# Kernel tuning notes

Measured on AMD Instinct MI355X. Metric: run time of the kernel, lower is better.

Reference implementation:

```python
import jax, jax.numpy as jnp
import numpy as np

SEQ, DM, NH, DH = 8192, 1024, 16, 64


def setup_inputs() -> dict:
    key = jax.random.key(0)
    k = jax.random.split(key, 8)
    return {
        "xs": jax.random.normal(k[0], (SEQ, DM), dtype=jnp.float32),
        "wq": jax.random.normal(k[1], (NH, DH, DM), dtype=jnp.float32),
        "wk": jax.random.normal(k[2], (NH, DH, DM), dtype=jnp.float32),
        "wv": jax.random.normal(k[3], (NH, DH, DM), dtype=jnp.float32),
        # MLP: Linear(NH*DH -> DM), gelu, Linear(DM -> NH*DH); eqx stores W as (out, in)
        "w1": jax.random.normal(k[4], (DM, NH * DH), dtype=jnp.float32) * 0.02,
        "b1": jnp.zeros((DM,), dtype=jnp.float32),
        "w2": jax.random.normal(k[5], (NH * DH, DM), dtype=jnp.float32) * 0.02,
        "b2": jnp.zeros((NH * DH,), dtype=jnp.float32),
    }


def _act(x):
    return jax.nn.elu(x) + 1.0


def reference(xs, wq, wk, wv, w1, b1, w2, b2):
    # project: (n_heads d_head d_model),(seq d_model) -> (seq n_heads d_head)
    q = jnp.einsum('hdm,sm->shd', wq, xs)
    k = jnp.einsum('hdm,sm->shd', wk, xs)
    v = jnp.einsum('hdm,sm->shd', wv, xs)

    def cell(state, qkv):
        s, z = state                      # s: (h, dk, dv), z: (h, dk)
        qt, kt, vt = qkv                  # each (h, d)
        kt = _act(kt)
        s = s + jnp.einsum('hk,hv->hkv', kt, vt)
        z = z + kt
        qa = _act(qt)
        # faithful to einops 'n_heads d_head_k d_head_v, n_heads d_head_q -> n_heads d_head_v'
        sq = jnp.einsum('hkv,hq->hv', s, qa)
        zq = jnp.einsum('hk,hq->h', z, qa)
        return (s, z), sq / zq[:, None]

    init = (jnp.zeros((NH, DH, DH), xs.dtype), jnp.zeros((NH, DH), xs.dtype))
    _, out = jax.lax.scan(cell, init, (q, k, v))   # out: (seq, h, d)
    out = out.reshape(SEQ, NH * DH)
    h = jax.nn.gelu(out @ w1.T + b1)
    return h @ w2.T + b2
```

## Files before the change

kernel.cpp:

```cpp
#include <hip/hip_runtime.h>
#include <hip/hip_bf16.h>

using bf16 = __hip_bfloat16;
typedef __attribute__((ext_vector_type(8))) short shortx8;
typedef __attribute__((ext_vector_type(4))) float f32x4;

#define SEQ 8192
#define DM 1024
#define NH 16
#define CHUNK 64
#define NC (SEQ / CHUNK)
#define NT (DM / 64)

__device__ __forceinline__ void load_lds16(const bf16* g, bf16* l) {
    __builtin_amdgcn_global_load_lds(
        (const __attribute__((address_space(1))) void*)g,
        (__attribute__((address_space(3))) void*)l, 16, 0, 0);
}

__device__ __forceinline__ unsigned ldsoff(const bf16* p) {
    return (unsigned)(unsigned long long)(__attribute__((address_space(3))) const void*)p;
}

__device__ __forceinline__ shortx8 dsr128(unsigned a) {
    shortx8 r;
    asm volatile("ds_read_b128 %0, %1" : "=v"(r) : "v"(a));
    return r;
}

__device__ __forceinline__ float bf2f(short s) {
    union { unsigned u; float f; } x;
    x.u = ((unsigned)(unsigned short)s) << 16;
    return x.f;
}

__global__ __launch_bounds__(256) void convert_all(const float* __restrict__ xs,
                                                   const float* __restrict__ wk,
                                                   const float* __restrict__ wv,
                                                   const float* __restrict__ w1,
                                                   const float* __restrict__ w2,
                                                   bf16* __restrict__ xsb,
                                                   bf16* __restrict__ wall) {
    const int b = blockIdx.x;
    const float* in;
    bf16* out;
    int blk;
    if (b < 8192) {
        in = xs; out = xsb; blk = b;
    } else {
        const int seg = (b - 8192) >> 10;
        blk = (b - 8192) & 1023;
        out = wall + (size_t)seg * DM * DM;
        if (seg == 0)      in = wk;
        else if (seg == 1) in = wv;
        else if (seg == 2) in = w1;
        else               in = w2;
    }
    size_t i = ((size_t)blk * 256 + threadIdx.x) * 4;
    float4 f = *(const float4*)(in + i);
    out[i + 0] = __float2bfloat16(f.x);
    out[i + 1] = __float2bfloat16(f.y);
    out[i + 2] = __float2bfloat16(f.z);
    out[i + 3] = __float2bfloat16(f.w);
}

__global__ __launch_bounds__(512, 2) void gemm256(const bf16* __restrict__ A,
                                                  const bf16* __restrict__ B,
                                                  void* __restrict__ Cv,
                                                  float* __restrict__ kappa,
                                                  int N) {
    __shared__ __align__(16) bf16 As[2][256][64];
    __shared__ __align__(16) bf16 Bs[2][256][64];

    const int tid = threadIdx.x;
    const int nwg = gridDim.x * gridDim.y;
    const int bid = blockIdx.x + blockIdx.y * gridDim.x;
    const int cpx = nwg >> 3;
    const int swz = (bid & 7) * cpx + (bid >> 3);
    const int ry  = swz % gridDim.y;
    const int rx  = swz / gridDim.y;
    const int bm  = ry * 256;
    const int bn  = rx * 256;

    const int wave = tid >> 6;
    const int lane = tid & 63;
    const int wr   = wave >> 2;
    const int wc   = wave & 3;
    const int quad = lane >> 4;
    const int m16  = lane & 15;
    const int r7   = m16 & 7;
    const int wr128 = wr * 128;
    const int wc64  = wc * 64;
    const int kp0 = ((quad ^ r7) * 8);
    const int kp1 = (((4 + quad) ^ r7) * 8);

    auto stageA = [&](int half, int kt) {
        #pragma unroll
        for (int it = 0; it < 2; ++it) {
            int s = it * 512 + tid;
            int row = s >> 3, pos = s & 7;
            int g = pos ^ (row & 7);
            load_lds16(A + (size_t)(bm + half * 128 + row) * DM + kt * 64 + g * 8,
                       &As[kt & 1][half * 128 + row][pos * 8]);
        }
    };
    auto stageB = [&](int half, int kt) {
        #pragma unroll
        for (int it = 0; it < 2; ++it) {
            int s = it * 512 + tid;
            int row = s >> 3, pos = s & 7;
            int g = pos ^ (row & 7);
            load_lds16(B + (size_t)(bn + half * 128 + row) * DM + kt * 64 + g * 8,
                       &Bs[kt & 1][half * 128 + row][pos * 8]);
        }
    };

    f32x4 acc[8][4];
    #pragma unroll
    for (int i = 0; i < 8; ++i)
        #pragma unroll
        for (int j = 0; j < 4; ++j)
            #pragma unroll
            for (int r = 0; r < 4; ++r) acc[i][j][r] = 0.f;

    stageA(0, 0); stageA(1, 0); stageB(0, 0); stageB(1, 0);
    stageB(0, 1); stageB(1, 1);
    asm volatile("s_waitcnt vmcnt(4)");
    __builtin_amdgcn_s_barrier();

    shortx8 af[4][2], blo[2][2], bhi[2][2];

    #pragma unroll 1
    for (int t = 0; t < NT; ++t) {
        const int sl = t & 1;
        if (t + 1 < NT) { stageA(0, t + 1); stageA(1, t + 1); }
        #pragma unroll
        for (int i = 0; i < 4; ++i) {
            af[i][0] = dsr128(ldsoff(&As[sl][wr128 + i * 16 + m16][kp0]));
            af[i][1] = dsr128(ldsoff(&As[sl][wr128 + i * 16 + m16][kp1]));
        }
        #pragma unroll
        for (int j = 0; j < 2; ++j) {
            blo[j][0] = dsr128(ldsoff(&Bs[sl][wc64 + j * 16 + m16][kp0]));
            blo[j][1] = dsr128(ldsoff(&Bs[sl][wc64 + j * 16 + m16][kp1]));
            bhi[j][0] = dsr128(ldsoff(&Bs[sl][wc64 + (j + 2) * 16 + m16][kp0]));
            bhi[j][1] = dsr128(ldsoff(&Bs[sl][wc64 + (j + 2) * 16 + m16][kp1]));
        }
        asm volatile("s_waitcnt lgkmcnt(0)");
        __builtin_amdgcn_sched_barrier(0);
        __builtin_amdgcn_s_setprio(1);
        #pragma unroll
        for (int i = 0; i < 4; ++i)
            #pragma unroll
            for (int j = 0; j < 2; ++j) {
                acc[i][j] = __builtin_amdgcn_mfma_f32_16x16x32_bf16(af[i][0], blo[j][0], acc[i][j], 0, 0, 0);
                acc[i][j] = __builtin_amdgcn_mfma_f32_16x16x32_bf16(af[i][1], blo[j][1], acc[i][j], 0, 0, 0);
                acc[i][j + 2] = __builtin_amdgcn_mfma_f32_16x16x32_bf16(af[i][0], bhi[j][0], acc[i][j + 2], 0, 0, 0);
                acc[i][j + 2] = __builtin_amdgcn_mfma_f32_16x16x32_bf16(af[i][1], bhi[j][1], acc[i][j + 2], 0, 0, 0);
            }
        __builtin_amdgcn_s_setprio(0);
        __builtin_amdgcn_s_barrier();

        if (t + 2 < NT) { stageB(0, t + 2); stageB(1, t + 2); }
        #pragma unroll
        for (int i = 0; i < 4; ++i) {
            af[i][0] = dsr128(ldsoff(&As[sl][wr128 + 64 + i * 16 + m16][kp0]));
            af[i][1] = dsr128(ldsoff(&As[sl][wr128 + 64 + i * 16 + m16][kp1]));
        }
        asm volatile("s_waitcnt lgkmcnt(0)");
        __builtin_amdgcn_sched_barrier(0);
        __builtin_amdgcn_s_setprio(1);
        #pragma unroll
        for (int i = 0; i < 4; ++i)
            #pragma unroll
            for (int j = 0; j < 2; ++j) {
                acc[4 + i][j] = __builtin_amdgcn_mfma_f32_16x16x32_bf16(af[i][0], blo[j][0], acc[4 + i][j], 0, 0, 0);
                acc[4 + i][j] = __builtin_amdgcn_mfma_f32_16x16x32_bf16(af[i][1], blo[j][1], acc[4 + i][j], 0, 0, 0);
                acc[4 + i][j + 2] = __builtin_amdgcn_mfma_f32_16x16x32_bf16(af[i][0], bhi[j][0], acc[4 + i][j + 2], 0, 0, 0);
                acc[4 + i][j + 2] = __builtin_amdgcn_mfma_f32_16x16x32_bf16(af[i][1], bhi[j][1], acc[4 + i][j + 2], 0, 0, 0);
            }
        __builtin_amdgcn_s_setprio(0);
        if (t + 2 < NT) {
            asm volatile("s_waitcnt vmcnt(4)");
        } else {
            asm volatile("s_waitcnt vmcnt(0)");
        }
        __builtin_amdgcn_s_barrier();
    }

    const int gcol0 = bn + wc64;
    if (gcol0 < DM) {
        const int h = gcol0 >> 6;
        #pragma unroll
        for (int i = 0; i < 8; ++i) {
            #pragma unroll
            for (int r = 0; r < 4; ++r) {
                float s = 0.f;
                #pragma unroll
                for (int j = 0; j < 4; ++j) {
                    float v = acc[i][j][r];
                    s += v > 0.f ? v + 1.f : __expf(v);
                }
                s += __shfl_xor(s, 1);
                s += __shfl_xor(s, 2);
                s += __shfl_xor(s, 4);
                s += __shfl_xor(s, 8);
                if (m16 == 0)
                    kappa[(size_t)h * SEQ + bm + wr128 + i * 16 + quad * 4 + r] = s;
            }
        }
    } else {
        bf16* vb = (bf16*)Cv;
        #pragma unroll
        for (int i = 0; i < 8; ++i) {
            int row0 = bm + wr128 + i * 16 + quad * 4;
            #pragma unroll
            for (int j = 0; j < 4; ++j) {
                int col = gcol0 - DM + j * 16 + m16;
                #pragma unroll
                for (int r = 0; r < 4; ++r)
                    vb[(size_t)(row0 + r) * DM + col] = __float2bfloat16(acc[i][j][r]);
            }
        }
    }
}

template <int MODE>
__global__ __launch_bounds__(512, 2) void gemm_mlp(const bf16* __restrict__ A,
                                                   const bf16* __restrict__ B,
                                                   void* __restrict__ Cv,
                                                   const float* __restrict__ bias,
                                                   int N) {
    __shared__ __align__(16) bf16 As[3][128][64];
    __shared__ __align__(16) bf16 Bs[2][256][64];

    const int tid = threadIdx.x;
    const int nwg = gridDim.x * gridDim.y;
    const int bid = blockIdx.x + blockIdx.y * gridDim.x;
    const int cpx = nwg >> 3;
    const int swz = (bid & 7) * cpx + (bid >> 3);
    const int ry  = swz % gridDim.y;
    const int rx  = swz / gridDim.y;
    const int bm  = ry * 128;
    const int bn  = rx * 256;

    const int wave = tid >> 6;
    const int lane = tid & 63;
    const int wr   = wave >> 2;
    const int wc   = wave & 3;
    const int quad = lane >> 4;
    const int m16  = lane & 15;
    const int r7   = m16 & 7;
    const int wr64 = wr * 64;
    const int wc64 = wc * 64;
    const int kp0 = ((quad ^ r7) * 8);
    const int kp1 = (((4 + quad) ^ r7) * 8);

    auto stageA = [&](int slot, int kt) {
        #pragma unroll
        for (int it = 0; it < 2; ++it) {
            int s = it * 512 + tid;
            int row = s >> 3, pos = s & 7;
            int g = pos ^ (row & 7);
            load_lds16(A + (size_t)(bm + row) * DM + kt * 64 + g * 8,
                       &As[slot][row][pos * 8]);
        }
    };
    auto stageB = [&](int half, int kt) {
        #pragma unroll
        for (int it = 0; it < 2; ++it) {
            int s = it * 512 + tid;
            int row = s >> 3, pos = s & 7;
            int g = pos ^ (row & 7);
            load_lds16(B + (size_t)(bn + half * 128 + row) * DM + kt * 64 + g * 8,
                       &Bs[kt & 1][half * 128 + row][pos * 8]);
        }
    };

    f32x4 acc[4][4];
    #pragma unroll
    for (int i = 0; i < 4; ++i)
        #pragma unroll
        for (int j = 0; j < 4; ++j)
            #pragma unroll
            for (int r = 0; r < 4; ++r) acc[i][j][r] = 0.f;

    stageA(0, 0); stageB(0, 0); stageB(1, 0);
    stageA(1, 1); stageB(0, 1); stageB(1, 1);
    asm volatile("s_waitcnt vmcnt(6)");
    __builtin_amdgcn_s_barrier();

    shortx8 af[4][2], bfr[4][2];

    int sl3 = 0;
    int st3 = 2;

    #pragma unroll 1
    for (int t = 0; t < NT; ++t) {
        const int slB = t & 1;
        if (t + 2 < NT) stageA(st3, t + 2);
        #pragma unroll
        for (int i = 0; i < 4; ++i) {
            af[i][0] = dsr128(ldsoff(&As[sl3][wr64 + i * 16 + m16][kp0]));
            af[i][1] = dsr128(ldsoff(&As[sl3][wr64 + i * 16 + m16][kp1]));
        }
        #pragma unroll
        for (int j = 0; j < 4; ++j) {
            bfr[j][0] = dsr128(ldsoff(&Bs[slB][wc64 + j * 16 + m16][kp0]));
            bfr[j][1] = dsr128(ldsoff(&Bs[slB][wc64 + j * 16 + m16][kp1]));
        }
        asm volatile("s_waitcnt lgkmcnt(0)");
        __builtin_amdgcn_sched_barrier(0);
        __builtin_amdgcn_s_setprio(1);
        #pragma unroll
        for (int i = 0; i < 4; ++i)
            #pragma unroll
            for (int j = 0; j < 2; ++j) {
                acc[i][j] = __builtin_amdgcn_mfma_f32_16x16x32_bf16(af[i][0], bfr[j][0], acc[i][j], 0, 0, 0);
                acc[i][j] = __builtin_amdgcn_mfma_f32_16x16x32_bf16(af[i][1], bfr[j][1], acc[i][j], 0, 0, 0);
            }
        __builtin_amdgcn_s_setprio(0);
        __builtin_amdgcn_s_barrier();

        if (t + 2 < NT) { stageB(0, t + 2); stageB(1, t + 2); }
        __builtin_amdgcn_s_setprio(1);
        #pragma unroll
        for (int i = 0; i < 4; ++i)
            #pragma unroll
            for (int j = 0; j < 2; ++j) {
                acc[i][j + 2] = __builtin_amdgcn_mfma_f32_16x16x32_bf16(af[i][0], bfr[j + 2][0], acc[i][j + 2], 0, 0, 0);
                acc[i][j + 2] = __builtin_amdgcn_mfma_f32_16x16x32_bf16(af[i][1], bfr[j + 2][1], acc[i][j + 2], 0, 0, 0);
            }
        __builtin_amdgcn_s_setprio(0);
        if (t + 2 < NT) {
            asm volatile("s_waitcnt vmcnt(6)");
        } else {
            asm volatile("s_waitcnt vmcnt(0)");
        }
        __builtin_amdgcn_s_barrier();
        sl3 = (sl3 == 2) ? 0 : sl3 + 1;
        st3 = (st3 == 2) ? 0 : st3 + 1;
    }

    #pragma unroll
    for (int i = 0; i < 4; ++i) {
        int row0 = bm + wr64 + i * 16 + quad * 4;
        #pragma unroll
        for (int j = 0; j < 4; ++j) {
            int col = bn + wc64 + j * 16 + m16;
            float bv = bias[col];
            #pragma unroll
            for (int r = 0; r < 4; ++r) {
                float v = acc[i][j][r] + bv;
                if (MODE == 2) {
                    float tt = tanhf(0.7978845608028654f * (v + 0.044715f * v * v * v));
                    ((bf16*)Cv)[(size_t)(row0 + r) * N + col] = __float2bfloat16(0.5f * v * (1.f + tt));
                } else {
                    ((float*)Cv)[(size_t)(row0 + r) * N + col] = v;
                }
            }
        }
    }
}

__global__ __launch_bounds__(256) void chunk_sums(const bf16* __restrict__ vb,
                                                  const float* __restrict__ kappa,
                                                  float* __restrict__ numbuf,
                                                  float* __restrict__ denbuf) {
    const int h = blockIdx.x;
    const int c = blockIdx.y * 4 + (threadIdx.x >> 6);
    const int v = threadIdx.x & 63;
    const size_t bidx = (size_t)h * NC + c;

    float kreg = kappa[(size_t)h * SEQ + c * 64 + v];
    float num = 0.f;
    const short* vrow = (const short*)vb + (size_t)(c * 64) * DM + h * 64 + v;
    #pragma unroll 8
    for (int t = 0; t < 64; ++t) {
        float kt = __shfl(kreg, t);
        num += kt * bf2f(vrow[0]);
        vrow += DM;
    }
    numbuf[bidx * 64 + v] = num;
    float d = kreg;
    #pragma unroll
    for (int off = 32; off > 0; off >>= 1) d += __shfl_xor(d, off);
    if (v == 0) denbuf[bidx] = d;
}

__global__ __launch_bounds__(256) void chunk_scan(const bf16* __restrict__ vb,
                                                  const float* __restrict__ kappa,
                                                  const float* __restrict__ numbuf,
                                                  const float* __restrict__ denbuf,
                                                  bf16* __restrict__ out) {
    const int h = blockIdx.x;
    const int c = blockIdx.y * 4 + (threadIdx.x >> 6);
    const int v = threadIdx.x & 63;
    const size_t bidx = (size_t)h * NC + c;

    float kreg = kappa[(size_t)h * SEQ + c * 64 + v];
    float num = numbuf[bidx * 64 + v];
    float den = denbuf[bidx];
    const short* vrow = (const short*)vb + (size_t)(c * 64) * DM + h * 64 + v;
    short* orow = (short*)out + (size_t)(c * 64) * DM + h * 64 + v;
    #pragma unroll 8
    for (int t = 0; t < 64; ++t) {
        float kt = __shfl(kreg, t);
        num += kt * bf2f(vrow[0]);
        den += kt;
        bf16 ob = __float2bfloat16(num / den);
        orow[0] = *(const short*)&ob;
        vrow += DM;
        orow += DM;
    }
}

__global__ __launch_bounds__(256) void prefix_state(float* __restrict__ numbuf,
                                                    float* __restrict__ denbuf) {
    const int h = blockIdx.x;
    const int wave = threadIdx.x >> 6;
    const int d = threadIdx.x & 63;
    __shared__ float tot[4][64];
    __shared__ float dtot[4];

    float val[32], dval[32];
    const int c0 = wave * 32;
    #pragma unroll
    for (int i = 0; i < 32; ++i) {
        size_t idx = (size_t)h * NC + c0 + i;
        val[i]  = numbuf[idx * 64 + d];
        dval[i] = denbuf[idx];
    }
    float run = 0.f, drun = 0.f;
    #pragma unroll
    for (int i = 0; i < 32; ++i) {
        float t = val[i];  val[i]  = run;  run  += t;
        float dt = dval[i]; dval[i] = drun; drun += dt;
    }
    tot[wave][d] = run;
    if (d == 0) dtot[wave] = drun;
    __syncthreads();
    float off = 0.f, doff = 0.f;
    for (int w = 0; w < wave; ++w) { off += tot[w][d]; doff += dtot[w]; }
    #pragma unroll
    for (int i = 0; i < 32; ++i) {
        size_t idx = (size_t)h * NC + c0 + i;
        numbuf[idx * 64 + d] = val[i] + off;
        if (d == 0) denbuf[idx] = dval[i] + doff;
    }
}

extern "C" void kernel_launch(void* const* d_in, const int* in_sizes, int n_in,
                              void* d_out, int out_size, void* d_ws, size_t ws_size,
                              hipStream_t stream) {
    const float* xs = (const float*)d_in[0];
    const float* wk = (const float*)d_in[2];
    const float* wv = (const float*)d_in[3];
    const float* w1 = (const float*)d_in[4];
    const float* b1 = (const float*)d_in[5];
    const float* w2 = (const float*)d_in[6];
    const float* b2 = (const float*)d_in[7];
    float* y = (float*)d_out;

    char* base = (char*)d_ws;
    size_t off = 0;
    auto alloc = [&](size_t b) -> char* {
        char* p = base + off;
        off += (b + 255) & ~(size_t)255;
        return p;
    };

    const size_t NMAT = (size_t)SEQ * DM;
    const size_t NW   = (size_t)DM * DM;
    bf16*  xsb    = (bf16*)alloc(NMAT * 2);
    bf16*  wall   = (bf16*)alloc(4 * NW * 2);
    bf16*  w1b    = wall + 2 * NW;
    bf16*  w2b    = wall + 3 * NW;
    bf16*  vb     = (bf16*)alloc(NMAT * 2);
    float* kappa  = (float*)alloc((size_t)NH * SEQ * 4);
    float* numbuf = (float*)alloc((size_t)NH * NC * 64 * 4);
    float* denbuf = (float*)alloc((size_t)NH * NC * 4);
    bf16*  outb   = (bf16*)alloc(NMAT * 2);
    bf16*  hb     = (bf16*)alloc(NMAT * 2);

    convert_all<<<8192 + 4 * 1024, 256, 0, stream>>>(xs, wk, wv, w1, w2,
                                                     xsb, wall);

    gemm256<<<dim3(2048 / 256, SEQ / 256), 512, 0, stream>>>(
        xsb, wall, vb, kappa, 2048);

    chunk_sums<<<dim3(NH, NC / 4), 256, 0, stream>>>(vb, kappa, numbuf, denbuf);
    prefix_state<<<NH, 256, 0, stream>>>(numbuf, denbuf);
    chunk_scan<<<dim3(NH, NC / 4), 256, 0, stream>>>(vb, kappa, numbuf, denbuf,
                                                     outb);

    gemm_mlp<2><<<dim3(DM / 256, SEQ / 128), 512, 0, stream>>>(
        outb, w1b, hb, b1, DM);
    gemm_mlp<3><<<dim3(DM / 256, SEQ / 128), 512, 0, stream>>>(
        hb, w2b, y, b2, DM);
}
```

Before: 205.9 us.

## Enlarge MLP GEMM tiles to 256x256 with double-buffered A and B

The two MLP GEMMs now use 256x256 output tiles instead of 128x256, so each wave computes a 128x64 sub-tile with 128 fp32 accumulator values. A drops from triple to double buffering with a one-step prefetch, and B fragments are reused across two A half-loads within each k-step. This raises arithmetic intensity per LDS and global load but halves the grid to 128 workgroups on a 256-CU part and increases register pressure under launch_bounds(512,2), which could cause spills or poor occupancy.

Result: slower. 233.8 us (+13.6%).

```diff
diff --git a/kernel.cpp b/kernel.cpp
--- a/kernel.cpp
+++ b/kernel.cpp
@@ -226,12 +226,11 @@
 }
 
 template <int MODE>
-__global__ __launch_bounds__(512, 2) void gemm_mlp(const bf16* __restrict__ A,
-                                                   const bf16* __restrict__ B,
-                                                   void* __restrict__ Cv,
-                                                   const float* __restrict__ bias,
-                                                   int N) {
-    __shared__ __align__(16) bf16 As[3][128][64];
+__global__ __launch_bounds__(512, 2) void gemm_mlp256(const bf16* __restrict__ A,
+                                                      const bf16* __restrict__ B,
+                                                      void* __restrict__ Cv,
+                                                      const float* __restrict__ bias) {
+    __shared__ __align__(16) bf16 As[2][256][64];
     __shared__ __align__(16) bf16 Bs[2][256][64];
 
     const int tid = threadIdx.x;
@@ -241,7 +240,7 @@
     const int swz = (bid & 7) * cpx + (bid >> 3);
     const int ry  = swz % gridDim.y;
     const int rx  = swz / gridDim.y;
-    const int bm  = ry * 128;
+    const int bm  = ry * 256;
     const int bn  = rx * 256;
 
     const int wave = tid >> 6;
@@ -251,19 +250,19 @@
     const int quad = lane >> 4;
     const int m16  = lane & 15;
     const int r7   = m16 & 7;
-    const int wr64 = wr * 64;
-    const int wc64 = wc * 64;
+    const int wr128 = wr * 128;
+    const int wc64  = wc * 64;
     const int kp0 = ((quad ^ r7) * 8);
     const int kp1 = (((4 + quad) ^ r7) * 8);
 
-    auto stageA = [&](int slot, int kt) {
+    auto stageA = [&](int half, int kt) {
         #pragma unroll
         for (int it = 0; it < 2; ++it) {
             int s = it * 512 + tid;
             int row = s >> 3, pos = s & 7;
             int g = pos ^ (row & 7);
-            load_lds16(A + (size_t)(bm + row) * DM + kt * 64 + g * 8,
-                       &As[slot][row][pos * 8]);
+            load_lds16(A + (size_t)(bm + half * 128 + row) * DM + kt * 64 + g * 8,
+                       &As[kt & 1][half * 128 + row][pos * 8]);
         }
     };
     auto stageB = [&](int half, int kt) {
@@ -277,37 +276,36 @@
         }
     };
 
-    f32x4 acc[4][4];
-    #pragma unroll
-    for (int i = 0; i < 4; ++i)
+    f32x4 acc[8][4];
+    #pragma unroll
+    for (int i = 0; i < 8; ++i)
         #pragma unroll
         for (int j = 0; j < 4; ++j)
             #pragma unroll
             for (int r = 0; r < 4; ++r) acc[i][j][r] = 0.f;
 
-    stageA(0, 0); stageB(0, 0); stageB(1, 0);
-    stageA(1, 1); stageB(0, 1); stageB(1, 1);
-    asm volatile("s_waitcnt vmcnt(6)");
+    stageA(0, 0); stageA(1, 0); stageB(0, 0); stageB(1, 0);
+    stageB(0, 1); stageB(1, 1);
+    asm volatile("s_waitcnt vmcnt(4)");
     __builtin_amdgcn_s_barrier();
 
-    shortx8 af[4][2], bfr[4][2];
-
-    int sl3 = 0;
-    int st3 = 2;
+    shortx8 af[4][2], blo[2][2], bhi[2][2];
 
     #pragma unroll 1
     for (int t = 0; t < NT; ++t) {
-        const int slB = t & 1;
-        if (t + 2 < NT) stageA(st3, t + 2);
+        const int sl = t & 1;
+        if (t + 1 < NT) { stageA(0, t + 1); stageA(1, t + 1); }
         #pragma unroll
         for (int i = 0; i < 4; ++i) {
-            af[i][0] = dsr128(ldsoff(&As[sl3][wr64 + i * 16 + m16][kp0]));
-            af[i][1] = dsr128(ldsoff(&As[sl3][wr64 + i * 16 + m16][kp1]));
-        }
-        #pragma unroll
-        for (int j = 0; j < 4; ++j) {
-            bfr[j][0] = dsr128(ldsoff(&Bs[slB][wc64 + j * 16 + m16][kp0]));
-            bfr[j][1] = dsr128(ldsoff(&Bs[slB][wc64 + j * 16 + m16][kp1]));
+            af[i][0] = dsr128(ldsoff(&As[sl][wr128 + i * 16 + m16][kp0]));
+            af[i][1] = dsr128(ldsoff(&As[sl][wr128 + i * 16 + m16][kp1]));
+        }
+        #pragma unroll
+        for (int j = 0; j < 2; ++j) {
+            blo[j][0] = dsr128(ldsoff(&Bs[sl][wc64 + j * 16 + m16][kp0]));
+            blo[j][1] = dsr128(ldsoff(&Bs[sl][wc64 + j * 16 + m16][kp1]));
+            bhi[j][0] = dsr128(ldsoff(&Bs[sl][wc64 + (j + 2) * 16 + m16][kp0]));
+            bhi[j][1] = dsr128(ldsoff(&Bs[sl][wc64 + (j + 2) * 16 + m16][kp1]));
         }
         asm volatile("s_waitcnt lgkmcnt(0)");
         __builtin_amdgcn_sched_barrier(0);
@@ -316,35 +314,44 @@
         for (int i = 0; i < 4; ++i)
             #pragma unroll
             for (int j = 0; j < 2; ++j) {
-                acc[i][j] = __builtin_amdgcn_mfma_f32_16x16x32_bf16(af[i][0], bfr[j][0], acc[i][j], 0, 0, 0);
-                acc[i][j] = __builtin_amdgcn_mfma_f32_16x16x32_bf16(af[i][1], bfr[j][1], acc[i][j], 0, 0, 0);
+                acc[i][j] = __builtin_amdgcn_mfma_f32_16x16x32_bf16(af[i][0], blo[j][0], acc[i][j], 0, 0, 0);
+                acc[i][j] = __builtin_amdgcn_mfma_f32_16x16x32_bf16(af[i][1], blo[j][1], acc[i][j], 0, 0, 0);
+                acc[i][j + 2] = __builtin_amdgcn_mfma_f32_16x16x32_bf16(af[i][0], bhi[j][0], acc[i][j + 2], 0, 0, 0);
+                acc[i][j + 2] = __builtin_amdgcn_mfma_f32_16x16x32_bf16(af[i][1], bhi[j][1], acc[i][j + 2], 0, 0, 0);
             }
         __builtin_amdgcn_s_setprio(0);
         __builtin_amdgcn_s_barrier();
 
         if (t + 2 < NT) { stageB(0, t + 2); stageB(1, t + 2); }
+        #pragma unroll
+        for (int i = 0; i < 4; ++i) {
+            af[i][0] = dsr128(ldsoff(&As[sl][wr128 + 64 + i * 16 + m16][kp0]));
+            af[i][1] = dsr128(ldsoff(&As[sl][wr128 + 64 + i * 16 + m16][kp1]));
+        }
+        asm volatile("s_waitcnt lgkmcnt(0)");
+        __builtin_amdgcn_sched_barrier(0);
         __builtin_amdgcn_s_setprio(1);
         #pragma unroll
         for (int i = 0; i < 4; ++i)
             #pragma unroll
             for (int j = 0; j < 2; ++j) {
-                acc[i][j + 2] = __builtin_amdgcn_mfma_f32_16x16x32_bf16(af[i][0], bfr[j + 2][0], acc[i][j + 2], 0, 0, 0);
-                acc[i][j + 2] = __builtin_amdgcn_mfma_f32_16x16x32_bf16(af[i][1], bfr[j + 2][1], acc[i][j + 2], 0, 0, 0);
+                acc[4 + i][j] = __builtin_amdgcn_mfma_f32_16x16x32_bf16(af[i][0], blo[j][0], acc[4 + i][j], 0, 0, 0);
+                acc[4 + i][j] = __builtin_amdgcn_mfma_f32_16x16x32_bf16(af[i][1], blo[j][1], acc[4 + i][j], 0, 0, 0);
+                acc[4 + i][j + 2] = __builtin_amdgcn_mfma_f32_16x16x32_bf16(af[i][0], bhi[j][0], acc[4 + i][j + 2], 0, 0, 0);
+                acc[4 + i][j + 2] = __builtin_amdgcn_mfma_f32_16x16x32_bf16(af[i][1], bhi[j][1], acc[4 + i][j + 2], 0, 0, 0);
             }
         __builtin_amdgcn_s_setprio(0);
         if (t + 2 < NT) {
-            asm volatile("s_waitcnt vmcnt(6)");
+            asm volatile("s_waitcnt vmcnt(4)");
         } else {
             asm volatile("s_waitcnt vmcnt(0)");
         }
         __builtin_amdgcn_s_barrier();
-        sl3 = (sl3 == 2) ? 0 : sl3 + 1;
-        st3 = (st3 == 2) ? 0 : st3 + 1;
-    }
-
-    #pragma unroll
-    for (int i = 0; i < 4; ++i) {
-        int row0 = bm + wr64 + i * 16 + quad * 4;
+    }
+
+    #pragma unroll
+    for (int i = 0; i < 8; ++i) {
+        int row0 = bm + wr128 + i * 16 + quad * 4;
         #pragma unroll
         for (int j = 0; j < 4; ++j) {
             int col = bn + wc64 + j * 16 + m16;
@@ -354,9 +361,9 @@
                 float v = acc[i][j][r] + bv;
                 if (MODE == 2) {
                     float tt = tanhf(0.7978845608028654f * (v + 0.044715f * v * v * v));
-                    ((bf16*)Cv)[(size_t)(row0 + r) * N + col] = __float2bfloat16(0.5f * v * (1.f + tt));
+                    ((bf16*)Cv)[(size_t)(row0 + r) * DM + col] = __float2bfloat16(0.5f * v * (1.f + tt));
                 } else {
-                    ((float*)Cv)[(size_t)(row0 + r) * N + col] = v;
+                    ((float*)Cv)[(size_t)(row0 + r) * DM + col] = v;
                 }
             }
         }
@@ -494,8 +501,8 @@
     chunk_scan<<<dim3(NH, NC / 4), 256, 0, stream>>>(vb, kappa, numbuf, denbuf,
                                                      outb);
 
-    gemm_mlp<2><<<dim3(DM / 256, SEQ / 128), 512, 0, stream>>>(
-        outb, w1b, hb, b1, DM);
-    gemm_mlp<3><<<dim3(DM / 256, SEQ / 128), 512, 0, stream>>>(
-        hb, w2b, y, b2, DM);
-}
+    gemm_mlp256<2><<<dim3(DM / 256, SEQ / 256), 512, 0, stream>>>(
+        outb, w1b, hb, b1);
+    gemm_mlp256<3><<<dim3(DM / 256, SEQ / 256), 512, 0, stream>>>(
+        hb, w2b, y, b2);
+}
```
